# Kernel tuning notes

Measured on AMD Instinct MI355X. Metric: run time of the kernel, lower is better.

## Reference

```python
import jax, jax.numpy as jnp
import numpy as np

S, N, F = 32, 512, 256        # systems, atoms per system, feature/charge channels
R_EXCL = 5.0                  # neighbor_list_options.cutoff -> exclusion_radius
BOX = 30.0                    # box edge for random positions (Angstrom-scale)


def setup_inputs() -> dict:
    key = jax.random.key(0)
    k1, k2, k3, k4 = jax.random.split(key, 4)
    positions = jax.random.uniform(k1, (S, N, 3), dtype=jnp.float32) * BOX
    features = jax.random.normal(k2, (S * N, F), dtype=jnp.float32)
    W = jax.random.normal(k3, (F, F), dtype=jnp.float32) / jnp.sqrt(F)
    b = jax.random.normal(k4, (F,), dtype=jnp.float32) * 0.01
    return {"positions": positions, "features": features, "W": W, "b": b}


def _pair_potential(d):
    # CoulombPotential(smearing=None, exclusion_radius=R_EXCL).from_dist:
    # v(r) = (1/r) * (1 - f_cut(r)),  f_cut = 0.5*(1 + cos(pi*r/R_EXCL)) for r < R_EXCL
    fcut = jnp.where(d < R_EXCL, 0.5 * (1.0 + jnp.cos(jnp.pi * d / R_EXCL)), 0.0)
    return (1.0 / d) * (1.0 - fcut)


def reference(positions, features, W, b):
    # charges_map: Linear(F, F)
    charges = features @ W.T + b                      # [S*N, F]
    q = charges.reshape(S, N, F)                      # per-system charges

    # all-pairs distances per system (torch.combinations path, both directions
    # accumulated by the half-neighbor-list Calculator)
    diff = positions[:, :, None, :] - positions[:, None, :, :]   # [S,N,N,3]
    d = jnp.sqrt(jnp.sum(diff * diff, axis=-1))                  # [S,N,N]
    eye = jnp.eye(N, dtype=bool)
    d_safe = jnp.where(eye, 1.0, d)
    v = jnp.where(eye, 0.0, _pair_potential(d_safe))             # [S,N,N]

    # V_i = 0.5 * sum_j v(r_ij) q_j  (torchpme energy convention E = sum_i q_i V_i)
    V = 0.5 * jnp.einsum('sij,sjf->sif', v, q)                   # [S,N,F]

    # module returns potential * charges, concatenated over systems
    return (V * q).reshape(S * N, F)
```

## Files before the change

### kernel.cpp

```cpp
#include <hip/hip_runtime.h>
#include <hip/hip_cooperative_groups.h>

#define SY 32
#define NA 512
#define FD 256

typedef __attribute__((ext_vector_type(8))) short bf16x8;
typedef __attribute__((ext_vector_type(4))) short bf16x4;
typedef __attribute__((ext_vector_type(4))) float f32x4;

static __device__ __forceinline__ short f2bf(float x) {
    union { float f; unsigned u; } v; v.f = x;
    unsigned r = v.u + 0x7fffu + ((v.u >> 16) & 1u);
    return (short)(r >> 16);
}
static __device__ __forceinline__ float bf2f(short x) {
    union { float f; unsigned u; } v;
    v.u = ((unsigned)(unsigned short)x) << 16;
    return v.f;
}

__global__ __launch_bounds__(512) void charges_mfma(
    const float* __restrict__ feat, const float* __restrict__ W,
    const float* __restrict__ b, float* __restrict__ qfp,
    short* __restrict__ qT)
{
    __shared__ __attribute__((aligned(16))) short sA[64 * 72];
    __shared__ __attribute__((aligned(16))) short sB[256 * 72];
    __shared__ __attribute__((aligned(16))) short tr[256 * 72];
    const int t    = threadIdx.x;
    const int i0   = blockIdx.x * 64;
    const int w    = t >> 6;
    const int lane = t & 63;
    const int n16  = lane & 15;
    const int quad = lane >> 4;

    f32x4 acc[4][2];
    #pragma unroll
    for (int a = 0; a < 4; ++a)
        #pragma unroll
        for (int c = 0; c < 2; ++c) acc[a][c] = (f32x4)0.0f;

    for (int k0 = 0; k0 < FD; k0 += 64) {
        #pragma unroll
        for (int m = 0; m < 2; ++m) {
            int lin = t + 512 * m;
            int i = lin >> 4, kq = lin & 15;
            float4 v = *(const float4*)&feat[(size_t)(i0 + i) * FD + k0 + 4 * kq];
            bf16x4 p; p[0] = f2bf(v.x); p[1] = f2bf(v.y);
                      p[2] = f2bf(v.z); p[3] = f2bf(v.w);
            *(bf16x4*)&sA[i * 72 + 4 * kq] = p;
        }
        #pragma unroll
        for (int m = 0; m < 8; ++m) {
            int lin = t + 512 * m;
            int f = lin >> 4, kq = lin & 15;
            float4 v = *(const float4*)&W[(size_t)f * FD + k0 + 4 * kq];
            bf16x4 p; p[0] = f2bf(v.x); p[1] = f2bf(v.y);
                      p[2] = f2bf(v.z); p[3] = f2bf(v.w);
            *(bf16x4*)&sB[f * 72 + 4 * kq] = p;
        }
        __syncthreads();

        #pragma unroll
        for (int ks = 0; ks < 64; ks += 32) {
            bf16x8 af[4], bfr[2];
            #pragma unroll
            for (int it = 0; it < 4; ++it)
                af[it] = *(const bf16x8*)&sA[(16 * it + n16) * 72 + ks + quad * 8];
            #pragma unroll
            for (int fb = 0; fb < 2; ++fb)
                bfr[fb] = *(const bf16x8*)&sB[(32 * w + 16 * fb + n16) * 72 + ks + quad * 8];
            #pragma unroll
            for (int it = 0; it < 4; ++it)
                #pragma unroll
                for (int fb = 0; fb < 2; ++fb)
                    acc[it][fb] = __builtin_amdgcn_mfma_f32_16x16x32_bf16(
                        af[it], bfr[fb], acc[it][fb], 0, 0, 0);
        }
        __syncthreads();
    }

    float bias[2];
    #pragma unroll
    for (int fb = 0; fb < 2; ++fb) bias[fb] = b[32 * w + 16 * fb + n16];

    if (qfp) {
        #pragma unroll
        for (int it = 0; it < 4; ++it)
            #pragma unroll
            for (int fb = 0; fb < 2; ++fb)
                #pragma unroll
                for (int r = 0; r < 4; ++r) {
                    int i = i0 + 16 * it + 4 * quad + r;
                    int f = 32 * w + 16 * fb + n16;
                    qfp[(size_t)i * FD + f] = acc[it][fb][r] + bias[fb];
                }
    }

    #pragma unroll
    for (int it = 0; it < 4; ++it)
        #pragma unroll
        for (int fb = 0; fb < 2; ++fb) {
            bf16x4 p;
            #pragma unroll
            for (int r = 0; r < 4; ++r) p[r] = f2bf(acc[it][fb][r] + bias[fb]);
            int f = 32 * w + 16 * fb + n16;
            *(bf16x4*)&tr[f * 72 + 16 * it + 4 * quad] = p;
        }
    __syncthreads();
    {
        short* qTs = qT + ((size_t)(i0 >> 9)) * FD * NA;
        const int ilb = i0 & 511;
        #pragma unroll
        for (int n = 0; n < 4; ++n) {
            int S = n * 512 + t;
            int f = S >> 3;
            int c = S & 7;
            uint4 v = *(const uint4*)&tr[f * 72 + c * 8];
            *(uint4*)&qTs[(size_t)f * NA + ilb + c * 8] = v;
        }
    }
}

__global__ __launch_bounds__(256) void lr_fast(
    const float* __restrict__ pos, float* __restrict__ gbuf,
    const short* __restrict__ qT)
{
    __shared__ float px[NA], py[NA], pz[NA];
    __shared__ __attribute__((aligned(16))) short sqb[FD * 64];
    __shared__ __attribute__((aligned(16))) short svb[32 * 64];

    const int blk = blockIdx.x;
    const int s   = blk & 31;
    const int i0  = (blk >> 5) * 32;
    const int t   = threadIdx.x;
    const int w    = t >> 6;
    const int lane = t & 63;
    const int n16  = lane & 15;
    const int quad = lane >> 4;

    for (int m = t; m < NA; m += 256) {
        const float* p = &pos[((size_t)s * NA + m) * 3];
        px[m] = p[0]; py[m] = p[1]; pz[m] = p[2];
    }

    f32x4 acc[2][4];
    #pragma unroll
    for (int a = 0; a < 2; ++a)
        #pragma unroll
        for (int c = 0; c < 4; ++c) acc[a][c] = (f32x4)0.0f;
    float qreg[2][4][4];

    const short* qTs = qT + (size_t)s * FD * NA;
    const int pi = t & 31;
    const int pc = t >> 5;
    const int gi = i0 + pi;

    __syncthreads();
    const float xi = px[gi], yi = py[gi], zi = pz[gi];

    for (int j0 = 0; j0 < NA; j0 += 64) {
        #pragma unroll
        for (int n = 0; n < 8; ++n) {
            int S  = n * 256 + t;
            int f  = S >> 3;
            int cs = S & 7;
            int c  = (cs - f) & 7;
            uint4 v = *(const uint4*)&qTs[(size_t)f * NA + j0 + c * 8];
            *(uint4*)&sqb[f * 64 + cs * 8] = v;
        }
        bf16x8 vrow;
        #pragma unroll
        for (int jj = 0; jj < 8; ++jj) {
            int gj = j0 + pc * 8 + jj;
            float dx = xi - px[gj];
            float dy = yi - py[gj];
            float dz = zi - pz[gj];
            float r2 = dx * dx + dy * dy + dz * dz;
            float inv = __builtin_amdgcn_rsqf(r2);
            float dd  = r2 * inv;
            float sn = __sinf(dd * 0.31415926535f);
            float om = (dd < 5.0f) ? sn * sn : 1.0f;
            float vv = (gi != gj) ? 0.5f * om * inv : 0.0f;
            vrow[jj] = f2bf(vv);
        }
        *(bf16x8*)&svb[pi * 64 + (((pc + pi) & 7) * 8)] = vrow;
        __syncthreads();

        if (j0 == (i0 & ~63)) {
            const int jb0 = i0 & 63;
            #pragma unroll
            for (int it = 0; it < 2; ++it)
                #pragma unroll
                for (int fb = 0; fb < 4; ++fb) {
                    int f = 64 * w + 16 * fb + n16;
                    #pragma unroll
                    for (int r = 0; r < 4; ++r) {
                        int jl = jb0 + 16 * it + 4 * quad + r;
                        int c  = jl >> 3, o = jl & 7;
                        qreg[it][fb][r] =
                            bf2f(sqb[f * 64 + (((c + f) & 7) * 8) + o]);
                    }
                }
        }

        bf16x8 af[2][2], bfr[2][4];
        #pragma unroll
        for (int it = 0; it < 2; ++it)
            #pragma unroll
            for (int kh = 0; kh < 2; ++kh) {
                int i = 16 * it + n16;
                int c = kh * 4 + quad;
                af[it][kh] = *(const bf16x8*)&svb[i * 64 + (((c + i) & 7) * 8)];
            }
        #pragma unroll
        for (int fb = 0; fb < 4; ++fb)
            #pragma unroll
            for (int kh = 0; kh < 2; ++kh) {
                int f = 64 * w + 16 * fb + n16;
                int c = kh * 4 + quad;
                bfr[kh][fb] = *(const bf16x8*)&sqb[f * 64 + (((c + f) & 7) * 8)];
            }
        #pragma unroll
        for (int kh = 0; kh < 2; ++kh)
            #pragma unroll
            for (int it = 0; it < 2; ++it)
                #pragma unroll
                for (int fb = 0; fb < 4; ++fb)
                    acc[it][fb] = __builtin_amdgcn_mfma_f32_16x16x32_bf16(
                        af[it][kh], bfr[kh][fb], acc[it][fb], 0, 0, 0);
        __syncthreads();
    }

    #pragma unroll
    for (int it = 0; it < 2; ++it)
        #pragma unroll
        for (int fb = 0; fb < 4; ++fb)
            #pragma unroll
            for (int r = 0; r < 4; ++r) {
                int i = i0 + 16 * it + 4 * quad + r;
                int f = 64 * w + 16 * fb + n16;
                size_t a = ((size_t)s * NA + i) * FD + f;
                gbuf[a] = acc[it][fb][r] * qreg[it][fb][r];
            }
}

__global__ __launch_bounds__(256) void lr_coop(
    const float* __restrict__ pos, float* __restrict__ gbuf)
{
    __shared__ float px[NA], py[NA], pz[NA];
    __shared__ __attribute__((aligned(16))) short svb[64 * 40];
    __shared__ __attribute__((aligned(16))) short sqb[FD * 40];

    const int blk = blockIdx.x;
    const int s   = blk & 31;
    const int i0  = (blk >> 5) * 64;
    const int t   = threadIdx.x;
    const int w    = t >> 6;
    const int lane = t & 63;
    const int n16  = lane & 15;
    const int quad = lane >> 4;

    for (int m = t; m < NA; m += 256) {
        const float* p = &pos[((size_t)s * NA + m) * 3];
        px[m] = p[0]; py[m] = p[1]; pz[m] = p[2];
    }

    f32x4 acc[4][4];
    #pragma unroll
    for (int a = 0; a < 4; ++a)
        #pragma unroll
        for (int c = 0; c < 4; ++c) acc[a][c] = (f32x4)0.0f;

    __syncthreads();

    const int fq  = t >> 2;
    const int jb  = t & 3;
    const int iv  = t & 63;
    const int jbv = t >> 6;
    const int gi  = i0 + iv;

    float4 rq[8];
    #pragma unroll
    for (int m = 0; m < 8; ++m)
        rq[m] = *(const float4*)&gbuf[((size_t)s * NA + 8 * jb + m) * FD + 4 * fq];

    for (int j0 = 0; j0 < NA; j0 += 32) {
        bf16x8 vrow;
        #pragma unroll
        for (int jj = 0; jj < 8; ++jj) {
            int gj = j0 + 8 * jbv + jj;
            float dx = px[gi] - px[gj];
            float dy = py[gi] - py[gj];
            float dz = pz[gi] - pz[gj];
            float dd = sqrtf(dx * dx + dy * dy + dz * dz);
            float om = (dd < 5.0f) ? 0.5f * (1.0f - __cosf(dd * 0.62831853071795f))
                                   : 1.0f;
            float vv = (gi != gj) ? (0.5f * om * __builtin_amdgcn_rcpf(dd)) : 0.0f;
            vrow[jj] = f2bf(vv);
        }
        bf16x8 rows[4];
        #pragma unroll
        for (int m = 0; m < 8; ++m) {
            rows[0][m] = f2bf(rq[m].x);
            rows[1][m] = f2bf(rq[m].y);
            rows[2][m] = f2bf(rq[m].z);
            rows[3][m] = f2bf(rq[m].w);
        }
        #pragma unroll
        for (int d = 0; d < 4; ++d) {
            int f = 4 * fq + d;
            int phys = (jb + (f >> 3)) & 3;
            *(bf16x8*)&sqb[f * 40 + phys * 8] = rows[d];
        }
        {
            int phys = (jbv + (iv >> 3)) & 3;
            *(bf16x8*)&svb[iv * 40 + phys * 8] = vrow;
        }
        {
            int jn = (j0 + 32) & (NA - 1);
            #pragma unroll
            for (int m = 0; m < 8; ++m)
                rq[m] = *(const float4*)&gbuf[((size_t)s * NA + jn + 8 * jb + m) * FD + 4 * fq];
        }
        __syncthreads();

        bf16x8 af[4], bfr[4];
        #pragma unroll
        for (int it = 0; it < 4; ++it) {
            int i = 16 * it + n16;
            int phys = (quad + (i >> 3)) & 3;
            af[it] = *(const bf16x8*)&svb[i * 40 + phys * 8];
        }
        #pragma unroll
        for (int fb = 0; fb < 4; ++fb) {
            int f = 16 * (4 * w + fb) + n16;
            int phys = (quad + (f >> 3)) & 3;
            bfr[fb] = *(const bf16x8*)&sqb[f * 40 + phys * 8];
        }
        #pragma unroll
        for (int it = 0; it < 4; ++it)
            #pragma unroll
            for (int fb = 0; fb < 4; ++fb)
                acc[it][fb] = __builtin_amdgcn_mfma_f32_16x16x32_bf16(
                    af[it], bfr[fb], acc[it][fb], 0, 0, 0);
        __syncthreads();
    }

    cooperative_groups::this_grid().sync();

    #pragma unroll
    for (int it = 0; it < 4; ++it)
        #pragma unroll
        for (int fb = 0; fb < 4; ++fb)
            #pragma unroll
            for (int r = 0; r < 4; ++r) {
                int i = i0 + 16 * it + 4 * quad + r;
                int f = 16 * (4 * w + fb) + n16;
                size_t a = ((size_t)s * NA + i) * FD + f;
                gbuf[a] = acc[it][fb][r] * gbuf[a];
            }
}

extern "C" void kernel_launch(void* const* d_in, const int* in_sizes, int n_in,
                              void* d_out, int out_size, void* d_ws, size_t ws_size,
                              hipStream_t stream) {
    const float* positions = (const float*)d_in[0];
    const float* features  = (const float*)d_in[1];
    const float* W         = (const float*)d_in[2];
    const float* b         = (const float*)d_in[3];
    float* gbuf = (float*)d_out;

    const size_t qT_bytes = (size_t)SY * NA * FD * sizeof(short);
    const bool fast = (ws_size >= qT_bytes);
    short* qT = fast ? (short*)d_ws : nullptr;

    if (fast) {
        charges_mfma<<<dim3(256), 512, 0, stream>>>(features, W, b, nullptr, qT);
        lr_fast<<<dim3(512), 256, 0, stream>>>(positions, gbuf, qT);
    } else {
        charges_mfma<<<dim3(256), 512, 0, stream>>>(features, W, b, gbuf,
                                                    (short*)d_out );
        void* args[] = {(void*)&positions, (void*)&gbuf};
        hipLaunchCooperativeKernel((void*)lr_coop, dim3(256), dim3(256),
                                   args, 0, stream);
    }
}
```

Measured before the change: 110.9 us.

## Double K-chunk to 128 and load charge tiles via direct global-to-LDS loads

The lr_fast kernel now processes 128 neighbor atoms per iteration instead of 64, halving the number of loop iterations and block barriers. The transposed charge tile is copied straight from global memory into LDS with global_load_lds 16-byte loads, skipping the trip through registers. Launch bounds now request two blocks per SM and the MFMA loop is reordered to stream B fragments per k-step. LDS use roughly doubles (about 80KB per block), which may limit occupancy. The swizzle relies on the per-wave contiguous layout that global_load_lds writes, so correctness depends on that addressing matching.

New measurement: 97.00 us. 12.5% less time.

```diff
diff --git a/kernel.cpp b/kernel.cpp
--- a/kernel.cpp
+++ b/kernel.cpp
@@ -18,6 +18,13 @@
     union { float f; unsigned u; } v;
     v.u = ((unsigned)(unsigned short)x) << 16;
     return v.f;
+}
+
+static __device__ __forceinline__ void gld16(const void* g, void* l) {
+    __builtin_amdgcn_global_load_lds(
+        (const __attribute__((address_space(1))) void*)g,
+        (__attribute__((address_space(3))) void*)l,
+        16, 0, 0);
 }
 
 __global__ __launch_bounds__(512) void charges_mfma(
@@ -123,13 +130,13 @@
     }
 }
 
-__global__ __launch_bounds__(256) void lr_fast(
+__global__ __launch_bounds__(256, 2) void lr_fast(
     const float* __restrict__ pos, float* __restrict__ gbuf,
     const short* __restrict__ qT)
 {
     __shared__ float px[NA], py[NA], pz[NA];
-    __shared__ __attribute__((aligned(16))) short sqb[FD * 64];
-    __shared__ __attribute__((aligned(16))) short svb[32 * 64];
+    __shared__ __attribute__((aligned(16))) short sqb[FD * 128];
+    __shared__ __attribute__((aligned(16))) short svb[32 * 128];
 
     const int blk = blockIdx.x;
     const int s   = blk & 31;
@@ -156,24 +163,25 @@
     const int pi = t & 31;
     const int pc = t >> 5;
     const int gi = i0 + pi;
+    const int wbase = t & ~63;
 
     __syncthreads();
     const float xi = px[gi], yi = py[gi], zi = pz[gi];
 
-    for (int j0 = 0; j0 < NA; j0 += 64) {
-        #pragma unroll
-        for (int n = 0; n < 8; ++n) {
-            int S  = n * 256 + t;
-            int f  = S >> 3;
-            int cs = S & 7;
-            int c  = (cs - f) & 7;
-            uint4 v = *(const uint4*)&qTs[(size_t)f * NA + j0 + c * 8];
-            *(uint4*)&sqb[f * 64 + cs * 8] = v;
-        }
-        bf16x8 vrow;
+    for (int j0 = 0; j0 < NA; j0 += 128) {
+        #pragma unroll
+        for (int n = 0; n < 16; ++n) {
+            int Sl = n * 256 + t;
+            int f  = Sl >> 4;
+            int cs = Sl & 15;
+            int c  = (cs - f) & 15;
+            gld16(&qTs[(size_t)f * NA + j0 + c * 8],
+                  &sqb[(n * 256 + wbase) * 8]);
+        }
+        bf16x8 vA, vB;
         #pragma unroll
         for (int jj = 0; jj < 8; ++jj) {
-            int gj = j0 + pc * 8 + jj;
+            int gj = j0 + pc * 16 + jj;
             float dx = xi - px[gj];
             float dy = yi - py[gj];
             float dz = zi - pz[gj];
@@ -183,13 +191,28 @@
             float sn = __sinf(dd * 0.31415926535f);
             float om = (dd < 5.0f) ? sn * sn : 1.0f;
             float vv = (gi != gj) ? 0.5f * om * inv : 0.0f;
-            vrow[jj] = f2bf(vv);
-        }
-        *(bf16x8*)&svb[pi * 64 + (((pc + pi) & 7) * 8)] = vrow;
-        __syncthreads();
-
-        if (j0 == (i0 & ~63)) {
-            const int jb0 = i0 & 63;
+            vA[jj] = f2bf(vv);
+        }
+        #pragma unroll
+        for (int jj = 0; jj < 8; ++jj) {
+            int gj = j0 + pc * 16 + 8 + jj;
+            float dx = xi - px[gj];
+            float dy = yi - py[gj];
+            float dz = zi - pz[gj];
+            float r2 = dx * dx + dy * dy + dz * dz;
+            float inv = __builtin_amdgcn_rsqf(r2);
+            float dd  = r2 * inv;
+            float sn = __sinf(dd * 0.31415926535f);
+            float om = (dd < 5.0f) ? sn * sn : 1.0f;
+            float vv = (gi != gj) ? 0.5f * om * inv : 0.0f;
+            vB[jj] = f2bf(vv);
+        }
+        *(bf16x8*)&svb[pi * 128 + (((2 * pc + pi) & 15) * 8)]     = vA;
+        *(bf16x8*)&svb[pi * 128 + (((2 * pc + 1 + pi) & 15) * 8)] = vB;
+        __syncthreads();
+
+        if (j0 == (i0 & ~127)) {
+            const int jb0 = i0 & 127;
             #pragma unroll
             for (int it = 0; it < 2; ++it)
                 #pragma unroll
@@ -200,36 +223,30 @@
                         int jl = jb0 + 16 * it + 4 * quad + r;
                         int c  = jl >> 3, o = jl & 7;
                         qreg[it][fb][r] =
-                            bf2f(sqb[f * 64 + (((c + f) & 7) * 8) + o]);
+                            bf2f(sqb[f * 128 + (((c + f) & 15) * 8) + o]);
                     }
                 }
         }
 
-        bf16x8 af[2][2], bfr[2][4];
-        #pragma unroll
-        for (int it = 0; it < 2; ++it)
-            #pragma unroll
-            for (int kh = 0; kh < 2; ++kh) {
-                int i = 16 * it + n16;
-                int c = kh * 4 + quad;
-                af[it][kh] = *(const bf16x8*)&svb[i * 64 + (((c + i) & 7) * 8)];
+        #pragma unroll
+        for (int kh = 0; kh < 4; ++kh) {
+            const int c = kh * 4 + quad;
+            bf16x8 a0 = *(const bf16x8*)&svb[n16 * 128 + (((c + n16) & 15) * 8)];
+            bf16x8 a1 = *(const bf16x8*)&svb[(16 + n16) * 128 + (((c + 16 + n16) & 15) * 8)];
+            bf16x8 bq[4];
+            #pragma unroll
+            for (int fb = 0; fb < 4; ++fb) {
+                int f = 64 * w + 16 * fb + n16;
+                bq[fb] = *(const bf16x8*)&sqb[f * 128 + (((c + f) & 15) * 8)];
             }
-        #pragma unroll
-        for (int fb = 0; fb < 4; ++fb)
-            #pragma unroll
-            for (int kh = 0; kh < 2; ++kh) {
-                int f = 64 * w + 16 * fb + n16;
-                int c = kh * 4 + quad;
-                bfr[kh][fb] = *(const bf16x8*)&sqb[f * 64 + (((c + f) & 7) * 8)];
+            #pragma unroll
+            for (int fb = 0; fb < 4; ++fb) {
+                acc[0][fb] = __builtin_amdgcn_mfma_f32_16x16x32_bf16(
+                    a0, bq[fb], acc[0][fb], 0, 0, 0);
+                acc[1][fb] = __builtin_amdgcn_mfma_f32_16x16x32_bf16(
+                    a1, bq[fb], acc[1][fb], 0, 0, 0);
             }
-        #pragma unroll
-        for (int kh = 0; kh < 2; ++kh)
-            #pragma unroll
-            for (int it = 0; it < 2; ++it)
-                #pragma unroll
-                for (int fb = 0; fb < 4; ++fb)
-                    acc[it][fb] = __builtin_amdgcn_mfma_f32_16x16x32_bf16(
-                        af[it][kh], bfr[kh][fb], acc[it][fb], 0, 0, 0);
+        }
         __syncthreads();
     }
 
```
